# Kernel optimization log

Hardware: AMD Instinct MI355X
Metric: run time of the kernel (lower is better)

Reference implementation:

```python
import jax, jax.numpy as jnp
import numpy as np

BETA = 0.25
EPS = 1e-10


def setup_inputs() -> dict:
    key = jax.random.key(0)
    k1, k2 = jax.random.split(key)
    x = jax.random.normal(k1, (32, 64, 64, 64), dtype=jnp.float32)  # [B, C=embed_dim, H, W]
    embeddings = jax.random.normal(k2, (64, 512), dtype=jnp.float32)  # [embed_dim, K]
    return {"x": x, "embeddings": embeddings}


def reference(x, embeddings):
    B, C, H, W = x.shape
    K = embeddings.shape[1]
    sg = jax.lax.stop_gradient

    z_e = jnp.transpose(x, (0, 2, 3, 1))          # [B, H, W, C]
    z_flat = z_e.reshape(-1, C)                    # [N, C]

    # Squared L2 distances to codebook: ||z||^2 + ||e||^2 - 2 z.e
    dists = (
        jnp.sum(z_flat * z_flat, axis=1, keepdims=True)
        + jnp.sum(embeddings * embeddings, axis=0)
        - 2.0 * (z_flat @ embeddings)
    )                                              # [N, K]
    idx = jnp.argmin(dists, axis=1)                # [N]

    # Direct gather instead of one-hot matmul (same math)
    quantized = embeddings.T[idx].reshape(z_e.shape)  # [B, H, W, C]

    e_latent_loss = jnp.mean((sg(quantized) - z_e) ** 2)
    q_latent_loss = jnp.mean((quantized - sg(z_e)) ** 2)
    loss = q_latent_loss + BETA * e_latent_loss

    # Straight-through estimator
    quantized_st = z_e + sg(quantized - z_e)

    # Perplexity via codebook usage histogram (== mean of one-hot encodings)
    N = idx.shape[0]
    counts = jnp.zeros((K,), dtype=jnp.float32).at[idx].add(1.0)
    avg_probs = counts / N
    perplexity = jnp.exp(-jnp.sum(avg_probs * jnp.log(avg_probs + EPS)))

    quantized_out = jnp.transpose(quantized_st, (0, 3, 1, 2))  # [B, C, H, W]
    encoding_indices = idx.reshape(B, H, W)
    return loss, quantized_out, perplexity, encoding_indices
```

## Files before the change

kernel.cpp:

```cpp
#include <hip/hip_runtime.h>


#define B_ 32
#define C_ 64
#define HW_ 4096
#define K_ 512
#define N_ (B_ * HW_)
#define NC_ ((long long)N_ * C_)
#define ROWS_ 64
#define NBLK_ (N_ / ROWS_)
#define HBLK_ 64

typedef __attribute__((ext_vector_type(8))) short short8;
typedef __attribute__((ext_vector_type(4))) float float4_t;


__device__ __forceinline__ unsigned short f2bf(float f) {
    unsigned u = __float_as_uint(f);
    u += 0x7fffu + ((u >> 16) & 1u);
    return (unsigned short)(u >> 16);
}
__device__ __forceinline__ float bf2f(unsigned short h) {
    return __uint_as_float(((unsigned)h) << 16);
}
__device__ __forceinline__ int offA(int r, int c) {
    return ((r >> 4) << 10) + ((c >> 3) << 7) + ((r & 15) << 3) + (c & 7);
}
__device__ __forceinline__ void merge2(float& m1, int& i1, float& m2,
                                       float om1, int oi1, float om2) {
    if (om1 < m1) { m2 = fminf(m1, om2); m1 = om1; i1 = oi1; }
    else          { m2 = fminf(m2, om1); }
}

__global__ __launch_bounds__(512) void vq_init(const float* __restrict__ emb,
                                               float* __restrict__ snmax_p,
                                               float* __restrict__ en,
                                               float* __restrict__ embT32,
                                               unsigned short* __restrict__ fBhi,
                                               unsigned short* __restrict__ fBlo) {
    __shared__ float smax[8];
    int k = threadIdx.x;
    if (blockIdx.x < 64) {
        int c = blockIdx.x;
        float e = emb[c * K_ + k];
        embT32[k * C_ + c] = e;
        float s = -2.0f * e;
        unsigned short hi = f2bf(s);
        unsigned short lo = f2bf(s - bf2f(hi));
        int kk   = c >> 5;
        int lane = (((c & 31) >> 3) << 4) + (k & 15);
        int fb   = ((k >> 5) << 2) + (((k >> 4) & 1) << 1) + kk;
        int off  = (fb << 9) + (lane << 3) + (c & 7);
        fBhi[off] = hi;
        fBlo[off] = lo;
    } else {
        float s = 0.f;
#pragma unroll
        for (int c = 0; c < C_; ++c) {
            float e = emb[c * K_ + k];
            s += e * e;
        }
        en[k] = s;
        float m = s;
#pragma unroll
        for (int off = 32; off > 0; off >>= 1)
            m = fmaxf(m, __shfl_down(m, off, 64));
        if ((k & 63) == 0) smax[k >> 6] = m;
        __syncthreads();
        if (k == 0) {
            float mm = smax[0];
#pragma unroll
            for (int w2 = 1; w2 < 8; ++w2) mm = fmaxf(mm, smax[w2]);
            *snmax_p = 4.0f * mm;
        }
    }
}

__global__ __launch_bounds__(256) void vq_argmin(const float* __restrict__ x,
                                                 const float* __restrict__ en_g,
                                                 const float* __restrict__ embT32,
                                                 const unsigned short* __restrict__ fBhi,
                                                 const unsigned short* __restrict__ fBlo,
                                                 const float* __restrict__ snmax_p,
                                                 float* __restrict__ out_q,
                                                 float* __restrict__ out_idx,
                                                 double* __restrict__ ssepart) {
    __shared__ unsigned short Ast[ROWS_ * C_];
    __shared__ float sEn[K_];
    __shared__ float znp[4 * ROWS_];
    __shared__ int   biarr[ROWS_];
    __shared__ int   flaglist[ROWS_];
    __shared__ float wsse[4];
    __shared__ int   nflag;

    const int t   = threadIdx.x;
    const int n0  = blockIdx.x * ROWS_;
    const int b   = n0 >> 12;
    const int hw0 = n0 & 4095;
    const float* xbase = x + ((size_t)b << 18) + hw0;

    if (t == 0) nflag = 0;
    sEn[t]       = en_g[t];
    sEn[256 + t] = en_g[256 + t];

    float v[16];
    float znacc = 0.f;
#pragma unroll
    for (int i = 0; i < 16; ++i) {
        int id = (i << 8) + t;
        int c = id >> 6;
        int r = id & 63;
        float val = xbase[((size_t)c << 12) + r];
        v[i] = val;
        znacc += val * val;
        Ast[offA(r, c)] = f2bf(val);
    }
    znp[((t >> 6) << 6) + (t & 63)] = znacc;
    __syncthreads();

    const int lane = t & 63;
    const int w    = t >> 6;
    const int ln15 = lane & 15;
    const int quad = lane >> 4;
    const float snm = *snmax_p;

    const int ab = (w << 10) + (quad << 7) + (ln15 << 3);
    short8 ah0 = *(const short8*)(Ast + ab);
    short8 ah1 = *(const short8*)(Ast + ab + 512);
    __syncthreads();

#pragma unroll
    for (int i = 0; i < 16; ++i) {
        int id = (i << 8) + t;
        int c = id >> 6;
        int r = id & 63;
        float val = v[i];
        unsigned short hi = f2bf(val);
        Ast[offA(r, c)] = f2bf(val - bf2f(hi));
    }
    __syncthreads();
    short8 al0 = *(const short8*)(Ast + ab);
    short8 al1 = *(const short8*)(Ast + ab + 512);

    float m1[4], m2[4];
    int   i1[4];
#pragma unroll
    for (int reg = 0; reg < 4; ++reg) {
        m1[reg] = 3.4e38f; m2[reg] = 3.4e38f; i1[reg] = 0;
    }

    for (int p = 0; p < 16; ++p) {
#pragma unroll
        for (int ct = 0; ct < 2; ++ct) {
            const int fbase = ((((p << 2) + (ct << 1)) << 9) + (lane << 3));
            short8 bh0 = *(const short8*)(fBhi + fbase);
            short8 bh1 = *(const short8*)(fBhi + fbase + 512);
            short8 bl0 = *(const short8*)(fBlo + fbase);
            short8 bl1 = *(const short8*)(fBlo + fbase + 512);
            float env = sEn[(p << 5) + (ct << 4) + ln15];
            int   idx = (p << 5) + (ct << 4) + ln15;
            float4_t a0 = {0.f, 0.f, 0.f, 0.f};
            float4_t a1 = {0.f, 0.f, 0.f, 0.f};
            a0 = __builtin_amdgcn_mfma_f32_16x16x32_bf16(al0, bh0, a0, 0, 0, 0);
            a1 = __builtin_amdgcn_mfma_f32_16x16x32_bf16(al1, bh1, a1, 0, 0, 0);
            a0 = __builtin_amdgcn_mfma_f32_16x16x32_bf16(ah0, bl0, a0, 0, 0, 0);
            a1 = __builtin_amdgcn_mfma_f32_16x16x32_bf16(ah1, bl1, a1, 0, 0, 0);
            a0 = __builtin_amdgcn_mfma_f32_16x16x32_bf16(ah0, bh0, a0, 0, 0, 0);
            a1 = __builtin_amdgcn_mfma_f32_16x16x32_bf16(ah1, bh1, a1, 0, 0, 0);
#pragma unroll
            for (int reg = 0; reg < 4; ++reg) {
                float vv = (a0[reg] + a1[reg]) + env;
                if (vv < m1[reg]) {
                    m2[reg] = m1[reg]; m1[reg] = vv; i1[reg] = idx;
                } else {
                    m2[reg] = fminf(m2[reg], vv);
                }
            }
        }
    }

#pragma unroll
    for (int reg = 0; reg < 4; ++reg) {
        float a1v = m1[reg], a2v = m2[reg];
        int   ai  = i1[reg];
#pragma unroll
        for (int s = 1; s < 16; s <<= 1) {
            float o1 = __shfl_xor(a1v, s, 16);
            int   oi = __shfl_xor(ai, s, 16);
            float o2 = __shfl_xor(a2v, s, 16);
            merge2(a1v, ai, a2v, o1, oi, o2);
        }
        if (ln15 == 0) {
            int row = (w << 4) + (quad << 2) + reg;
            float znr = znp[row] + znp[64 + row] + znp[128 + row] + znp[192 + row];
            float W = 1.4e-4f * __builtin_sqrtf(znr * snm) + 1e-3f;
            biarr[row] = ai;
            if (a2v > a1v + W) {
                out_idx[n0 + row] = (float)ai;
            } else {
                int pos = atomicAdd(&nflag, 1);
                flaglist[pos] = row;
            }
        }
    }
    __syncthreads();

    int nf = nflag;
    for (int f = w; f < nf; f += 4) {
        int r = flaglist[f];
        float zl = xbase[((size_t)lane << 12) + r];
        float d[8];
#pragma unroll
        for (int j = 0; j < 8; ++j) d[j] = 0.f;
        for (int c4 = 0; c4 < 16; ++c4) {
            float z0 = __shfl(zl, (c4 << 2) + 0, 64);
            float z1 = __shfl(zl, (c4 << 2) + 1, 64);
            float z2 = __shfl(zl, (c4 << 2) + 2, 64);
            float z3 = __shfl(zl, (c4 << 2) + 3, 64);
#pragma unroll
            for (int j = 0; j < 8; ++j) {
                float4_t e = *(const float4_t*)(embT32 + ((((lane << 3) + j) << 6) + (c4 << 2)));
                d[j] = fmaf(z0, e[0], d[j]);
                d[j] = fmaf(z1, e[1], d[j]);
                d[j] = fmaf(z2, e[2], d[j]);
                d[j] = fmaf(z3, e[3], d[j]);
            }
        }
        float znr = znp[r] + znp[64 + r] + znp[128 + r] + znp[192 + r];
        float best = 3.4e38f;
        int   bidx = 0;
#pragma unroll
        for (int j = 0; j < 8; ++j) {
            int k = (lane << 3) + j;
            float dist = (znr + sEn[k]) - 2.f * d[j];
            if (dist < best) { best = dist; bidx = k; }
        }
#pragma unroll
        for (int off = 32; off > 0; off >>= 1) {
            float ov = __shfl_down(best, off, 64);
            int   oi = __shfl_down(bidx, off, 64);
            if (ov < best || (ov == best && oi < bidx)) { best = ov; bidx = oi; }
        }
        if (lane == 0) {
            biarr[r] = bidx;
            out_idx[n0 + r] = (float)bidx;
        }
    }
    __syncthreads();

    const int myrow = (w << 4) + ln15;
    const int code  = biarr[myrow];
    const float* eb = embT32 + (code << 6) + (quad << 3);
    float4_t e0 = *(const float4_t*)(eb);
    float4_t e1 = *(const float4_t*)(eb + 4);
    float4_t e2 = *(const float4_t*)(eb + 32);
    float4_t e3 = *(const float4_t*)(eb + 36);
    float* qrow = out_q + ((size_t)b << 18) + hw0 + myrow;
    float sacc = 0.f;
#pragma unroll
    for (int j = 0; j < 4; ++j) {
        int c0 = (quad << 3) + j;
        int c1 = (quad << 3) + 4 + j;
        float zA = bf2f((unsigned short)ah0[j])     + bf2f((unsigned short)al0[j]);
        float zB = bf2f((unsigned short)ah0[4 + j]) + bf2f((unsigned short)al0[4 + j]);
        float dA = e0[j] - zA, dB = e1[j] - zB;
        sacc += dA * dA + dB * dB;
        qrow[(size_t)c0 << 12] = e0[j];
        qrow[(size_t)c1 << 12] = e1[j];
        float zC = bf2f((unsigned short)ah1[j])     + bf2f((unsigned short)al1[j]);
        float zD = bf2f((unsigned short)ah1[4 + j]) + bf2f((unsigned short)al1[4 + j]);
        float dC = e2[j] - zC, dD = e3[j] - zD;
        sacc += dC * dC + dD * dD;
        qrow[(size_t)(32 + c0) << 12] = e2[j];
        qrow[(size_t)(32 + c1) << 12] = e3[j];
    }
#pragma unroll
    for (int off = 32; off > 0; off >>= 1)
        sacc += __shfl_down(sacc, off, 64);
    if (lane == 0) wsse[w] = sacc;
    __syncthreads();
    if (t == 0)
        ssepart[blockIdx.x] = (double)wsse[0] + (double)wsse[1]
                            + (double)wsse[2] + (double)wsse[3];
}

__global__ __launch_bounds__(256) void vq_hist(const float* __restrict__ out_idx,
                                               int* __restrict__ histpart) {
    __shared__ int h[K_];
    int t = threadIdx.x;
    h[t] = 0; h[t + 256] = 0;
    __syncthreads();
    const float* ip = out_idx + blockIdx.x * (N_ / HBLK_);
#pragma unroll
    for (int i = 0; i < (N_ / HBLK_) / 256; ++i) {
        int k = (int)ip[(i << 8) + t];
        atomicAdd(&h[k], 1);
    }
    __syncthreads();
    histpart[blockIdx.x * K_ + t]       = h[t];
    histpart[blockIdx.x * K_ + 256 + t] = h[t + 256];
}

__global__ __launch_bounds__(512) void vq_final(const int* __restrict__ histpart,
                                                const double* __restrict__ ssepart,
                                                float* __restrict__ out_loss,
                                                float* __restrict__ out_perp) {
    __shared__ float  wsf[8];
    __shared__ double wsd[8];
    int t = threadIdx.x;
    int hsum = 0;
#pragma unroll 8
    for (int b = 0; b < HBLK_; ++b)
        hsum += histpart[b * K_ + t];
    float p = (float)hsum / (float)N_;
    float s = p * logf(p + 1e-10f);
    double d = ssepart[t] + ssepart[t + 512] + ssepart[t + 1024] + ssepart[t + 1536];
#pragma unroll
    for (int off = 32; off > 0; off >>= 1) {
        s += __shfl_down(s, off, 64);
        d += __shfl_down(d, off, 64);
    }
    if ((t & 63) == 0) { wsf[t >> 6] = s; wsd[t >> 6] = d; }
    __syncthreads();
    if (t == 0) {
        float  S = 0.f;
        double D = 0.0;
#pragma unroll
        for (int w = 0; w < 8; ++w) { S += wsf[w]; D += wsd[w]; }
        *out_perp = expf(-S);
        *out_loss = (float)(1.25 * D / (double)NC_);
    }
}

extern "C" void kernel_launch(void* const* d_in, const int* in_sizes, int n_in,
                              void* d_out, int out_size, void* d_ws, size_t ws_size,
                              hipStream_t stream) {
    const float* x   = (const float*)d_in[0];
    const float* emb = (const float*)d_in[1];

    float* out      = (float*)d_out;
    float* out_loss = out;
    float* out_q    = out + 1;
    float* out_perp = out + 1 + (size_t)N_ * C_;
    float* out_idx  = out + 2 + (size_t)N_ * C_;

    char* ws = (char*)d_ws;
    float*          snmax_p  = (float*)(ws + 56);
    float*          en       = (float*)(ws + 2112);
    float*          embT32   = (float*)(ws + 4160);
    unsigned short* fBhi     = (unsigned short*)(ws + 135232);
    unsigned short* fBlo     = (unsigned short*)(ws + 200768);
    int*            histpart = (int*)(ws + 135232);
    double*         ssepart  = (double*)(ws + 266304);

    vq_init<<<65, 512, 0, stream>>>(emb, snmax_p, en, embT32, fBhi, fBlo);
    vq_argmin<<<NBLK_, 256, 0, stream>>>(x, en, embT32, fBhi, fBlo, snmax_p,
                                         out_q, out_idx, ssepart);
    vq_hist<<<HBLK_, 256, 0, stream>>>(out_idx, histpart);
    vq_final<<<1, 512, 0, stream>>>(histpart, ssepart, out_loss, out_perp);
}
```

Measured before the change: 154.6 us.

## Fuse histogram and final reduction into argmin kernel via last-block pattern

Removes the separate histogram and finalize kernels. Each block now atomically accumulates its SSE into a global double, and the last block to finish builds the codebook histogram and writes loss and perplexity. The MFMA loop is also restructured to prefetch the next codebook fragments a step ahead, adds a fourth lo*lo product term, seeds the accumulator with the codebook norms, and tightens the ambiguity margin so fewer rows fall back to exact fp32 rescoring. The cost is a serial tail where one block scans all 131072 indices, plus an extra MFMA per tile.

Measured after the change: 337.4 us. 2.18x slower.

```diff
diff --git a/kernel.cpp b/kernel.cpp
--- a/kernel.cpp
+++ b/kernel.cpp
@@ -9,7 +9,6 @@
 #define NC_ ((long long)N_ * C_)
 #define ROWS_ 64
 #define NBLK_ (N_ / ROWS_)
-#define HBLK_ 64
 
 typedef __attribute__((ext_vector_type(8))) short short8;
 typedef __attribute__((ext_vector_type(4))) float float4_t;
@@ -33,6 +32,8 @@
 }
 
 __global__ __launch_bounds__(512) void vq_init(const float* __restrict__ emb,
+                                               double* __restrict__ sse,
+                                               int* __restrict__ done,
                                                float* __restrict__ snmax_p,
                                                float* __restrict__ en,
                                                float* __restrict__ embT32,
@@ -54,6 +55,7 @@
         fBhi[off] = hi;
         fBlo[off] = lo;
     } else {
+        if (k == 0) { *sse = 0.0; *done = 0; }
         float s = 0.f;
 #pragma unroll
         for (int c = 0; c < C_; ++c) {
@@ -76,22 +78,27 @@
     }
 }
 
-__global__ __launch_bounds__(256) void vq_argmin(const float* __restrict__ x,
-                                                 const float* __restrict__ en_g,
-                                                 const float* __restrict__ embT32,
-                                                 const unsigned short* __restrict__ fBhi,
-                                                 const unsigned short* __restrict__ fBlo,
-                                                 const float* __restrict__ snmax_p,
-                                                 float* __restrict__ out_q,
-                                                 float* __restrict__ out_idx,
-                                                 double* __restrict__ ssepart) {
+__global__ __launch_bounds__(256) void vq_fused(const float* __restrict__ x,
+                                                const float* __restrict__ en_g,
+                                                const float* __restrict__ embT32,
+                                                const unsigned short* __restrict__ fBhi,
+                                                const unsigned short* __restrict__ fBlo,
+                                                const float* __restrict__ snmax_p,
+                                                float* __restrict__ out_q,
+                                                float* __restrict__ out_idx,
+                                                float* __restrict__ out_loss,
+                                                float* __restrict__ out_perp,
+                                                double* __restrict__ sse_g,
+                                                int* __restrict__ done) {
     __shared__ unsigned short Ast[ROWS_ * C_];
     __shared__ float sEn[K_];
     __shared__ float znp[4 * ROWS_];
     __shared__ int   biarr[ROWS_];
     __shared__ int   flaglist[ROWS_];
+    __shared__ int   h[K_];
     __shared__ float wsse[4];
     __shared__ int   nflag;
+    __shared__ int   islast;
 
     const int t   = threadIdx.x;
     const int n0  = blockIdx.x * ROWS_;
@@ -149,32 +156,40 @@
         m1[reg] = 3.4e38f; m2[reg] = 3.4e38f; i1[reg] = 0;
     }
 
-    for (int p = 0; p < 16; ++p) {
-#pragma unroll
-        for (int ct = 0; ct < 2; ++ct) {
-            const int fbase = ((((p << 2) + (ct << 1)) << 9) + (lane << 3));
-            short8 bh0 = *(const short8*)(fBhi + fbase);
-            short8 bh1 = *(const short8*)(fBhi + fbase + 512);
-            short8 bl0 = *(const short8*)(fBlo + fbase);
-            short8 bl1 = *(const short8*)(fBlo + fbase + 512);
-            float env = sEn[(p << 5) + (ct << 4) + ln15];
-            int   idx = (p << 5) + (ct << 4) + ln15;
-            float4_t a0 = {0.f, 0.f, 0.f, 0.f};
-            float4_t a1 = {0.f, 0.f, 0.f, 0.f};
-            a0 = __builtin_amdgcn_mfma_f32_16x16x32_bf16(al0, bh0, a0, 0, 0, 0);
-            a1 = __builtin_amdgcn_mfma_f32_16x16x32_bf16(al1, bh1, a1, 0, 0, 0);
-            a0 = __builtin_amdgcn_mfma_f32_16x16x32_bf16(ah0, bl0, a0, 0, 0, 0);
-            a1 = __builtin_amdgcn_mfma_f32_16x16x32_bf16(ah1, bl1, a1, 0, 0, 0);
-            a0 = __builtin_amdgcn_mfma_f32_16x16x32_bf16(ah0, bh0, a0, 0, 0, 0);
-            a1 = __builtin_amdgcn_mfma_f32_16x16x32_bf16(ah1, bh1, a1, 0, 0, 0);
-#pragma unroll
-            for (int reg = 0; reg < 4; ++reg) {
-                float vv = (a0[reg] + a1[reg]) + env;
-                if (vv < m1[reg]) {
-                    m2[reg] = m1[reg]; m1[reg] = vv; i1[reg] = idx;
-                } else {
-                    m2[reg] = fminf(m2[reg], vv);
-                }
+    short8 nb0 = *(const short8*)(fBhi + (lane << 3));
+    short8 nb1 = *(const short8*)(fBhi + (lane << 3) + 512);
+    short8 nb2 = *(const short8*)(fBlo + (lane << 3));
+    short8 nb3 = *(const short8*)(fBlo + (lane << 3) + 512);
+
+#pragma unroll 2
+    for (int it = 0; it < 32; ++it) {
+        short8 bh0 = nb0, bh1 = nb1, bl0 = nb2, bl1 = nb3;
+        if (it < 31) {
+            const int nfb = ((it + 1) << 10) + (lane << 3);
+            nb0 = *(const short8*)(fBhi + nfb);
+            nb1 = *(const short8*)(fBhi + nfb + 512);
+            nb2 = *(const short8*)(fBlo + nfb);
+            nb3 = *(const short8*)(fBlo + nfb + 512);
+        }
+        float env = sEn[(it << 4) + ln15];
+        int   idx = (it << 4) + ln15;
+        float4_t a0 = {env, env, env, env};
+        float4_t a1 = {0.f, 0.f, 0.f, 0.f};
+        a0 = __builtin_amdgcn_mfma_f32_16x16x32_bf16(al0, bl0, a0, 0, 0, 0);
+        a1 = __builtin_amdgcn_mfma_f32_16x16x32_bf16(al1, bl1, a1, 0, 0, 0);
+        a0 = __builtin_amdgcn_mfma_f32_16x16x32_bf16(al0, bh0, a0, 0, 0, 0);
+        a1 = __builtin_amdgcn_mfma_f32_16x16x32_bf16(al1, bh1, a1, 0, 0, 0);
+        a0 = __builtin_amdgcn_mfma_f32_16x16x32_bf16(ah0, bl0, a0, 0, 0, 0);
+        a1 = __builtin_amdgcn_mfma_f32_16x16x32_bf16(ah1, bl1, a1, 0, 0, 0);
+        a0 = __builtin_amdgcn_mfma_f32_16x16x32_bf16(ah0, bh0, a0, 0, 0, 0);
+        a1 = __builtin_amdgcn_mfma_f32_16x16x32_bf16(ah1, bh1, a1, 0, 0, 0);
+#pragma unroll
+        for (int reg = 0; reg < 4; ++reg) {
+            float vv = a0[reg] + a1[reg];
+            if (vv < m1[reg]) {
+                m2[reg] = m1[reg]; m1[reg] = vv; i1[reg] = idx;
+            } else {
+                m2[reg] = fminf(m2[reg], vv);
             }
         }
     }
@@ -193,10 +208,12 @@
         if (ln15 == 0) {
             int row = (w << 4) + (quad << 2) + reg;
             float znr = znp[row] + znp[64 + row] + znp[128 + row] + znp[192 + row];
-            float W = 1.4e-4f * __builtin_sqrtf(znr * snm) + 1e-3f;
+            float S = __builtin_sqrtf(znr * snm);
+            float W = 6.5e-5f * S + 3e-6f * (znr + snm) + 1e-4f;
             biarr[row] = ai;
             if (a2v > a1v + W) {
-                out_idx[n0 + row] = (float)ai;
+                __hip_atomic_store(&out_idx[n0 + row], (float)ai,
+                                   __ATOMIC_RELAXED, __HIP_MEMORY_SCOPE_AGENT);
             } else {
                 int pos = atomicAdd(&nflag, 1);
                 flaglist[pos] = row;
@@ -243,7 +260,8 @@
         }
         if (lane == 0) {
             biarr[r] = bidx;
-            out_idx[n0 + r] = (float)bidx;
+            __hip_atomic_store(&out_idx[n0 + r], (float)bidx,
+                               __ATOMIC_RELAXED, __HIP_MEMORY_SCOPE_AGENT);
         }
     }
     __syncthreads();
@@ -279,56 +297,42 @@
         sacc += __shfl_down(sacc, off, 64);
     if (lane == 0) wsse[w] = sacc;
     __syncthreads();
-    if (t == 0)
-        ssepart[blockIdx.x] = (double)wsse[0] + (double)wsse[1]
-                            + (double)wsse[2] + (double)wsse[3];
-}
-
-__global__ __launch_bounds__(256) void vq_hist(const float* __restrict__ out_idx,
-                                               int* __restrict__ histpart) {
-    __shared__ int h[K_];
-    int t = threadIdx.x;
-    h[t] = 0; h[t + 256] = 0;
-    __syncthreads();
-    const float* ip = out_idx + blockIdx.x * (N_ / HBLK_);
-#pragma unroll
-    for (int i = 0; i < (N_ / HBLK_) / 256; ++i) {
-        int k = (int)ip[(i << 8) + t];
-        atomicAdd(&h[k], 1);
-    }
-    __syncthreads();
-    histpart[blockIdx.x * K_ + t]       = h[t];
-    histpart[blockIdx.x * K_ + 256 + t] = h[t + 256];
-}
-
-__global__ __launch_bounds__(512) void vq_final(const int* __restrict__ histpart,
-                                                const double* __restrict__ ssepart,
-                                                float* __restrict__ out_loss,
-                                                float* __restrict__ out_perp) {
-    __shared__ float  wsf[8];
-    __shared__ double wsd[8];
-    int t = threadIdx.x;
-    int hsum = 0;
-#pragma unroll 8
-    for (int b = 0; b < HBLK_; ++b)
-        hsum += histpart[b * K_ + t];
-    float p = (float)hsum / (float)N_;
-    float s = p * logf(p + 1e-10f);
-    double d = ssepart[t] + ssepart[t + 512] + ssepart[t + 1024] + ssepart[t + 1536];
-#pragma unroll
-    for (int off = 32; off > 0; off >>= 1) {
-        s += __shfl_down(s, off, 64);
-        d += __shfl_down(d, off, 64);
-    }
-    if ((t & 63) == 0) { wsf[t >> 6] = s; wsd[t >> 6] = d; }
-    __syncthreads();
+
     if (t == 0) {
-        float  S = 0.f;
-        double D = 0.0;
-#pragma unroll
-        for (int w = 0; w < 8; ++w) { S += wsf[w]; D += wsd[w]; }
-        *out_perp = expf(-S);
-        *out_loss = (float)(1.25 * D / (double)NC_);
+        double bs = (double)wsse[0] + (double)wsse[1]
+                  + (double)wsse[2] + (double)wsse[3];
+        atomicAdd(sse_g, bs);
+        __threadfence();
+        islast = (atomicAdd(done, 1) == NBLK_ - 1);
+    }
+    __syncthreads();
+    if (islast) {
+        __threadfence();
+        h[t] = 0; h[t + 256] = 0;
+        __syncthreads();
+        for (int i = 0; i < N_ / 256; ++i) {
+            float fv = __hip_atomic_load(&out_idx[(i << 8) + t],
+                                         __ATOMIC_RELAXED, __HIP_MEMORY_SCOPE_AGENT);
+            atomicAdd(&h[(int)fv], 1);
+        }
+        __syncthreads();
+        float s = 0.f;
+#pragma unroll
+        for (int j = 0; j < 2; ++j) {
+            float pp = (float)h[t + (j << 8)] / (float)N_;
+            s += pp * logf(pp + 1e-10f);
+        }
+#pragma unroll
+        for (int off = 32; off > 0; off >>= 1)
+            s += __shfl_down(s, off, 64);
+        if (lane == 0) wsse[w] = s;
+        __syncthreads();
+        if (t == 0) {
+            float S2 = wsse[0] + wsse[1] + wsse[2] + wsse[3];
+            double sv = atomicAdd(sse_g, 0.0);
+            out_perp[0] = expf(-S2);
+            out_loss[0] = (float)(1.25 * sv / (double)NC_);
+        }
     }
 }
 
@@ -345,17 +349,16 @@
     float* out_idx  = out + 2 + (size_t)N_ * C_;
 
     char* ws = (char*)d_ws;
-    float*          snmax_p  = (float*)(ws + 56);
-    float*          en       = (float*)(ws + 2112);
-    float*          embT32   = (float*)(ws + 4160);
-    unsigned short* fBhi     = (unsigned short*)(ws + 135232);
-    unsigned short* fBlo     = (unsigned short*)(ws + 200768);
-    int*            histpart = (int*)(ws + 135232);
-    double*         ssepart  = (double*)(ws + 266304);
-
-    vq_init<<<65, 512, 0, stream>>>(emb, snmax_p, en, embT32, fBhi, fBlo);
-    vq_argmin<<<NBLK_, 256, 0, stream>>>(x, en, embT32, fBhi, fBlo, snmax_p,
-                                         out_q, out_idx, ssepart);
-    vq_hist<<<HBLK_, 256, 0, stream>>>(out_idx, histpart);
-    vq_final<<<1, 512, 0, stream>>>(histpart, ssepart, out_loss, out_perp);
-}
+    double*         sse     = (double*)(ws + 0);
+    int*            done    = (int*)(ws + 8);
+    float*          snmax_p = (float*)(ws + 56);
+    float*          en      = (float*)(ws + 2112);
+    float*          embT32  = (float*)(ws + 4160);
+    unsigned short* fBhi    = (unsigned short*)(ws + 135232);
+    unsigned short* fBlo    = (unsigned short*)(ws + 200768);
+
+    vq_init<<<65, 512, 0, stream>>>(emb, sse, done, snmax_p, en, embT32, fBhi, fBlo);
+    vq_fused<<<NBLK_, 256, 0, stream>>>(x, en, embT32, fBhi, fBlo, snmax_p,
+                                        out_q, out_idx, out_loss, out_perp,
+                                        sse, done);
+}
```

## Double rows per block, stage codebook in LDS, fold histogram into tail kernel

Applied to the files above, without the earlier changes.

Each argmin block now handles 128 rows as two row tiles per wave, so every codebook fragment is reused twice. The codebook fragments are staged through a double-buffered LDS ring with register prefetch instead of being read straight from global memory. A fourth low-by-low MFMA term is added, the codebook norm is seeded into the accumulator, and the tie-break threshold is tightened. The fallback exact-distance pass reads the original embedding layout, and the separate histogram and final kernels are merged into one single-block tail kernel. The risks are a serial 131k-element histogram in that single block, more register pressure from the launch-bounds hint, and a tighter threshold that could mis-flag near-tie rows.

Result: slower. 196.2 us (+26.9%).

```diff
diff --git a/kernel.cpp b/kernel.cpp
--- a/kernel.cpp
+++ b/kernel.cpp
@@ -7,9 +7,8 @@
 #define K_ 512
 #define N_ (B_ * HW_)
 #define NC_ ((long long)N_ * C_)
-#define ROWS_ 64
+#define ROWS_ 128
 #define NBLK_ (N_ / ROWS_)
-#define HBLK_ 64
 
 typedef __attribute__((ext_vector_type(8))) short short8;
 typedef __attribute__((ext_vector_type(4))) float float4_t;
@@ -76,25 +75,26 @@
     }
 }
 
-__global__ __launch_bounds__(256) void vq_argmin(const float* __restrict__ x,
-                                                 const float* __restrict__ en_g,
-                                                 const float* __restrict__ embT32,
-                                                 const unsigned short* __restrict__ fBhi,
-                                                 const unsigned short* __restrict__ fBlo,
-                                                 const float* __restrict__ snmax_p,
-                                                 float* __restrict__ out_q,
-                                                 float* __restrict__ out_idx,
-                                                 double* __restrict__ ssepart) {
-    __shared__ unsigned short Ast[ROWS_ * C_];
+__global__ __launch_bounds__(256, 4) void vq_argmin(const float* __restrict__ x,
+                                                    const float* __restrict__ emb,
+                                                    const float* __restrict__ en_g,
+                                                    const float* __restrict__ embT32,
+                                                    const unsigned short* __restrict__ fBhi,
+                                                    const unsigned short* __restrict__ fBlo,
+                                                    const float* __restrict__ snmax_p,
+                                                    float* __restrict__ out_q,
+                                                    float* __restrict__ out_idx,
+                                                    double* __restrict__ ssepart) {
+    __shared__ unsigned short SBuf[8192];
     __shared__ float sEn[K_];
-    __shared__ float znp[4 * ROWS_];
+    __shared__ float znp[256];
     __shared__ int   biarr[ROWS_];
     __shared__ int   flaglist[ROWS_];
     __shared__ float wsse[4];
     __shared__ int   nflag;
 
     const int t   = threadIdx.x;
-    const int n0  = blockIdx.x * ROWS_;
+    const int n0  = blockIdx.x << 7;
     const int b   = n0 >> 12;
     const int hw0 = n0 & 4095;
     const float* xbase = x + ((size_t)b << 18) + hw0;
@@ -103,19 +103,19 @@
     sEn[t]       = en_g[t];
     sEn[256 + t] = en_g[256 + t];
 
-    float v[16];
+    float v[32];
     float znacc = 0.f;
 #pragma unroll
-    for (int i = 0; i < 16; ++i) {
+    for (int i = 0; i < 32; ++i) {
         int id = (i << 8) + t;
-        int c = id >> 6;
-        int r = id & 63;
+        int c = id >> 7;
+        int r = id & 127;
         float val = xbase[((size_t)c << 12) + r];
         v[i] = val;
         znacc += val * val;
-        Ast[offA(r, c)] = f2bf(val);
-    }
-    znp[((t >> 6) << 6) + (t & 63)] = znacc;
+        SBuf[offA(r, c)] = f2bf(val);
+    }
+    znp[((t >> 7) << 7) + (t & 127)] = znacc;
     __syncthreads();
 
     const int lane = t & 63;
@@ -124,115 +124,152 @@
     const int quad = lane >> 4;
     const float snm = *snmax_p;
 
-    const int ab = (w << 10) + (quad << 7) + (ln15 << 3);
-    short8 ah0 = *(const short8*)(Ast + ab);
-    short8 ah1 = *(const short8*)(Ast + ab + 512);
-    __syncthreads();
-
-#pragma unroll
-    for (int i = 0; i < 16; ++i) {
+    short8 ah[2][2], al[2][2];
+    int abof[2];
+#pragma unroll
+    for (int rtl = 0; rtl < 2; ++rtl) {
+        abof[rtl] = (((w << 1) + rtl) << 10) + (quad << 7) + (ln15 << 3);
+        ah[rtl][0] = *(const short8*)(SBuf + abof[rtl]);
+        ah[rtl][1] = *(const short8*)(SBuf + abof[rtl] + 512);
+    }
+    __syncthreads();
+
+    uint4 ph = ((const uint4*)fBhi)[t];
+    uint4 pl = ((const uint4*)fBlo)[t];
+
+#pragma unroll
+    for (int i = 0; i < 32; ++i) {
         int id = (i << 8) + t;
-        int c = id >> 6;
-        int r = id & 63;
+        int c = id >> 7;
+        int r = id & 127;
         float val = v[i];
         unsigned short hi = f2bf(val);
-        Ast[offA(r, c)] = f2bf(val - bf2f(hi));
-    }
-    __syncthreads();
-    short8 al0 = *(const short8*)(Ast + ab);
-    short8 al1 = *(const short8*)(Ast + ab + 512);
-
-    float m1[4], m2[4];
-    int   i1[4];
-#pragma unroll
-    for (int reg = 0; reg < 4; ++reg) {
-        m1[reg] = 3.4e38f; m2[reg] = 3.4e38f; i1[reg] = 0;
-    }
-
-    for (int p = 0; p < 16; ++p) {
-#pragma unroll
-        for (int ct = 0; ct < 2; ++ct) {
-            const int fbase = ((((p << 2) + (ct << 1)) << 9) + (lane << 3));
-            short8 bh0 = *(const short8*)(fBhi + fbase);
-            short8 bh1 = *(const short8*)(fBhi + fbase + 512);
-            short8 bl0 = *(const short8*)(fBlo + fbase);
-            short8 bl1 = *(const short8*)(fBlo + fbase + 512);
-            float env = sEn[(p << 5) + (ct << 4) + ln15];
-            int   idx = (p << 5) + (ct << 4) + ln15;
-            float4_t a0 = {0.f, 0.f, 0.f, 0.f};
-            float4_t a1 = {0.f, 0.f, 0.f, 0.f};
-            a0 = __builtin_amdgcn_mfma_f32_16x16x32_bf16(al0, bh0, a0, 0, 0, 0);
-            a1 = __builtin_amdgcn_mfma_f32_16x16x32_bf16(al1, bh1, a1, 0, 0, 0);
-            a0 = __builtin_amdgcn_mfma_f32_16x16x32_bf16(ah0, bl0, a0, 0, 0, 0);
-            a1 = __builtin_amdgcn_mfma_f32_16x16x32_bf16(ah1, bl1, a1, 0, 0, 0);
-            a0 = __builtin_amdgcn_mfma_f32_16x16x32_bf16(ah0, bh0, a0, 0, 0, 0);
-            a1 = __builtin_amdgcn_mfma_f32_16x16x32_bf16(ah1, bh1, a1, 0, 0, 0);
-#pragma unroll
-            for (int reg = 0; reg < 4; ++reg) {
-                float vv = (a0[reg] + a1[reg]) + env;
-                if (vv < m1[reg]) {
-                    m2[reg] = m1[reg]; m1[reg] = vv; i1[reg] = idx;
-                } else {
-                    m2[reg] = fminf(m2[reg], vv);
+        SBuf[offA(r, c)] = f2bf(val - bf2f(hi));
+    }
+    __syncthreads();
+#pragma unroll
+    for (int rtl = 0; rtl < 2; ++rtl) {
+        al[rtl][0] = *(const short8*)(SBuf + abof[rtl]);
+        al[rtl][1] = *(const short8*)(SBuf + abof[rtl] + 512);
+    }
+    __syncthreads();
+
+    {
+        uint4* dst = (uint4*)SBuf;
+        dst[t]       = ph;
+        dst[256 + t] = pl;
+    }
+    __syncthreads();
+
+    float m1[2][4], m2[2][4];
+    int   i1[2][4];
+#pragma unroll
+    for (int rtl = 0; rtl < 2; ++rtl)
+#pragma unroll
+        for (int reg = 0; reg < 4; ++reg) {
+            m1[rtl][reg] = 3.4e38f; m2[rtl][reg] = 3.4e38f; i1[rtl][reg] = 0;
+        }
+
+    for (int cch = 0; cch < 16; ++cch) {
+        const int d = cch & 1;
+        if (cch < 15) {
+            ph = ((const uint4*)fBhi)[((cch + 1) << 8) + t];
+            pl = ((const uint4*)fBlo)[((cch + 1) << 8) + t];
+        }
+        const unsigned short* Bb = SBuf + (d << 12);
+#pragma unroll
+        for (int q = 0; q < 2; ++q) {
+            const unsigned short* Bh = Bb + (q << 10);
+            const unsigned short* Bl = Bb + 2048 + (q << 10);
+            short8 bh0 = *(const short8*)(Bh + (lane << 3));
+            short8 bh1 = *(const short8*)(Bh + 512 + (lane << 3));
+            short8 bl0 = *(const short8*)(Bl + (lane << 3));
+            short8 bl1 = *(const short8*)(Bl + 512 + (lane << 3));
+            const int it  = (cch << 1) + q;
+            const float env = sEn[(it << 4) + ln15];
+            const int   idx = (it << 4) + ln15;
+#pragma unroll
+            for (int rtl = 0; rtl < 2; ++rtl) {
+                float4_t a0 = {env, env, env, env};
+                float4_t a1 = {0.f, 0.f, 0.f, 0.f};
+                a0 = __builtin_amdgcn_mfma_f32_16x16x32_bf16(al[rtl][0], bl0, a0, 0, 0, 0);
+                a1 = __builtin_amdgcn_mfma_f32_16x16x32_bf16(al[rtl][1], bl1, a1, 0, 0, 0);
+                a0 = __builtin_amdgcn_mfma_f32_16x16x32_bf16(al[rtl][0], bh0, a0, 0, 0, 0);
+                a1 = __builtin_amdgcn_mfma_f32_16x16x32_bf16(al[rtl][1], bh1, a1, 0, 0, 0);
+                a0 = __builtin_amdgcn_mfma_f32_16x16x32_bf16(ah[rtl][0], bl0, a0, 0, 0, 0);
+                a1 = __builtin_amdgcn_mfma_f32_16x16x32_bf16(ah[rtl][1], bl1, a1, 0, 0, 0);
+                a0 = __builtin_amdgcn_mfma_f32_16x16x32_bf16(ah[rtl][0], bh0, a0, 0, 0, 0);
+                a1 = __builtin_amdgcn_mfma_f32_16x16x32_bf16(ah[rtl][1], bh1, a1, 0, 0, 0);
+#pragma unroll
+                for (int reg = 0; reg < 4; ++reg) {
+                    float vv = a0[reg] + a1[reg];
+                    if (vv < m1[rtl][reg]) {
+                        m2[rtl][reg] = m1[rtl][reg]; m1[rtl][reg] = vv; i1[rtl][reg] = idx;
+                    } else {
+                        m2[rtl][reg] = fminf(m2[rtl][reg], vv);
+                    }
                 }
             }
         }
-    }
-
-#pragma unroll
-    for (int reg = 0; reg < 4; ++reg) {
-        float a1v = m1[reg], a2v = m2[reg];
-        int   ai  = i1[reg];
-#pragma unroll
-        for (int s = 1; s < 16; s <<= 1) {
-            float o1 = __shfl_xor(a1v, s, 16);
-            int   oi = __shfl_xor(ai, s, 16);
-            float o2 = __shfl_xor(a2v, s, 16);
-            merge2(a1v, ai, a2v, o1, oi, o2);
-        }
-        if (ln15 == 0) {
-            int row = (w << 4) + (quad << 2) + reg;
-            float znr = znp[row] + znp[64 + row] + znp[128 + row] + znp[192 + row];
-            float W = 1.4e-4f * __builtin_sqrtf(znr * snm) + 1e-3f;
-            biarr[row] = ai;
-            if (a2v > a1v + W) {
-                out_idx[n0 + row] = (float)ai;
-            } else {
-                int pos = atomicAdd(&nflag, 1);
-                flaglist[pos] = row;
+        __syncthreads();
+        if (cch < 15) {
+            uint4* dst = (uint4*)SBuf + ((d ^ 1) << 9);
+            dst[t]       = ph;
+            dst[256 + t] = pl;
+        }
+        __syncthreads();
+    }
+
+#pragma unroll
+    for (int rtl = 0; rtl < 2; ++rtl)
+#pragma unroll
+        for (int reg = 0; reg < 4; ++reg) {
+            float a1v = m1[rtl][reg], a2v = m2[rtl][reg];
+            int   ai  = i1[rtl][reg];
+#pragma unroll
+            for (int s = 1; s < 16; s <<= 1) {
+                float o1 = __shfl_xor(a1v, s, 16);
+                int   oi = __shfl_xor(ai, s, 16);
+                float o2 = __shfl_xor(a2v, s, 16);
+                merge2(a1v, ai, a2v, o1, oi, o2);
             }
-        }
-    }
+            if (ln15 == 0) {
+                int row = (((w << 1) + rtl) << 4) + (quad << 2) + reg;
+                float znr = znp[row] + znp[128 + row];
+                float S = __builtin_sqrtf(znr * snm);
+                float W = 6.5e-5f * S + 3e-6f * (znr + snm) + 1e-4f;
+                biarr[row] = ai;
+                if (a2v > a1v + W) {
+                    out_idx[n0 + row] = (float)ai;
+                } else {
+                    int pos = atomicAdd(&nflag, 1);
+                    flaglist[pos] = row;
+                }
+            }
+        }
     __syncthreads();
 
     int nf = nflag;
     for (int f = w; f < nf; f += 4) {
         int r = flaglist[f];
         float zl = xbase[((size_t)lane << 12) + r];
-        float d[8];
-#pragma unroll
-        for (int j = 0; j < 8; ++j) d[j] = 0.f;
-        for (int c4 = 0; c4 < 16; ++c4) {
-            float z0 = __shfl(zl, (c4 << 2) + 0, 64);
-            float z1 = __shfl(zl, (c4 << 2) + 1, 64);
-            float z2 = __shfl(zl, (c4 << 2) + 2, 64);
-            float z3 = __shfl(zl, (c4 << 2) + 3, 64);
-#pragma unroll
-            for (int j = 0; j < 8; ++j) {
-                float4_t e = *(const float4_t*)(embT32 + ((((lane << 3) + j) << 6) + (c4 << 2)));
-                d[j] = fmaf(z0, e[0], d[j]);
-                d[j] = fmaf(z1, e[1], d[j]);
-                d[j] = fmaf(z2, e[2], d[j]);
-                d[j] = fmaf(z3, e[3], d[j]);
-            }
-        }
-        float znr = znp[r] + znp[64 + r] + znp[128 + r] + znp[192 + r];
+        float dd[8];
+#pragma unroll
+        for (int j = 0; j < 8; ++j) dd[j] = 0.f;
+        for (int c = 0; c < C_; ++c) {
+            float zc = __shfl(zl, c, 64);
+            const float* ep = emb + (c << 9);
+#pragma unroll
+            for (int j = 0; j < 8; ++j)
+                dd[j] = fmaf(zc, ep[(j << 6) + lane], dd[j]);
+        }
+        float znr = znp[r] + znp[128 + r];
         float best = 3.4e38f;
         int   bidx = 0;
 #pragma unroll
         for (int j = 0; j < 8; ++j) {
-            int k = (lane << 3) + j;
-            float dist = (znr + sEn[k]) - 2.f * d[j];
+            int k = (j << 6) + lane;
+            float dist = (znr + sEn[k]) - 2.f * dd[j];
             if (dist < best) { best = dist; bidx = k; }
         }
 #pragma unroll
@@ -248,31 +285,34 @@
     }
     __syncthreads();
 
-    const int myrow = (w << 4) + ln15;
-    const int code  = biarr[myrow];
-    const float* eb = embT32 + (code << 6) + (quad << 3);
-    float4_t e0 = *(const float4_t*)(eb);
-    float4_t e1 = *(const float4_t*)(eb + 4);
-    float4_t e2 = *(const float4_t*)(eb + 32);
-    float4_t e3 = *(const float4_t*)(eb + 36);
-    float* qrow = out_q + ((size_t)b << 18) + hw0 + myrow;
     float sacc = 0.f;
 #pragma unroll
-    for (int j = 0; j < 4; ++j) {
-        int c0 = (quad << 3) + j;
-        int c1 = (quad << 3) + 4 + j;
-        float zA = bf2f((unsigned short)ah0[j])     + bf2f((unsigned short)al0[j]);
-        float zB = bf2f((unsigned short)ah0[4 + j]) + bf2f((unsigned short)al0[4 + j]);
-        float dA = e0[j] - zA, dB = e1[j] - zB;
-        sacc += dA * dA + dB * dB;
-        qrow[(size_t)c0 << 12] = e0[j];
-        qrow[(size_t)c1 << 12] = e1[j];
-        float zC = bf2f((unsigned short)ah1[j])     + bf2f((unsigned short)al1[j]);
-        float zD = bf2f((unsigned short)ah1[4 + j]) + bf2f((unsigned short)al1[4 + j]);
-        float dC = e2[j] - zC, dD = e3[j] - zD;
-        sacc += dC * dC + dD * dD;
-        qrow[(size_t)(32 + c0) << 12] = e2[j];
-        qrow[(size_t)(32 + c1) << 12] = e3[j];
+    for (int rtl = 0; rtl < 2; ++rtl) {
+        const int myrow = (((w << 1) + rtl) << 4) + ln15;
+        const int code  = biarr[myrow];
+        const float* eb = embT32 + (code << 6) + (quad << 3);
+        float4_t e0 = *(const float4_t*)(eb);
+        float4_t e1 = *(const float4_t*)(eb + 4);
+        float4_t e2 = *(const float4_t*)(eb + 32);
+        float4_t e3 = *(const float4_t*)(eb + 36);
+        float* qrow = out_q + ((size_t)b << 18) + hw0 + myrow;
+#pragma unroll
+        for (int j = 0; j < 4; ++j) {
+            int c0 = (quad << 3) + j;
+            int c1 = (quad << 3) + 4 + j;
+            float zA = bf2f((unsigned short)ah[rtl][0][j])     + bf2f((unsigned short)al[rtl][0][j]);
+            float zB = bf2f((unsigned short)ah[rtl][0][4 + j]) + bf2f((unsigned short)al[rtl][0][4 + j]);
+            float dA = e0[j] - zA, dB = e1[j] - zB;
+            sacc += dA * dA + dB * dB;
+            qrow[(size_t)c0 << 12] = e0[j];
+            qrow[(size_t)c1 << 12] = e1[j];
+            float zC = bf2f((unsigned short)ah[rtl][1][j])     + bf2f((unsigned short)al[rtl][1][j]);
+            float zD = bf2f((unsigned short)ah[rtl][1][4 + j]) + bf2f((unsigned short)al[rtl][1][4 + j]);
+            float dC = e2[j] - zC, dD = e3[j] - zD;
+            sacc += dC * dC + dD * dD;
+            qrow[(size_t)(32 + c0) << 12] = e2[j];
+            qrow[(size_t)(32 + c1) << 12] = e3[j];
+        }
     }
 #pragma unroll
     for (int off = 32; off > 0; off >>= 1)
@@ -284,37 +324,25 @@
                             + (double)wsse[2] + (double)wsse[3];
 }
 
-__global__ __launch_bounds__(256) void vq_hist(const float* __restrict__ out_idx,
-                                               int* __restrict__ histpart) {
-    __shared__ int h[K_];
-    int t = threadIdx.x;
-    h[t] = 0; h[t + 256] = 0;
-    __syncthreads();
-    const float* ip = out_idx + blockIdx.x * (N_ / HBLK_);
-#pragma unroll
-    for (int i = 0; i < (N_ / HBLK_) / 256; ++i) {
-        int k = (int)ip[(i << 8) + t];
-        atomicAdd(&h[k], 1);
-    }
-    __syncthreads();
-    histpart[blockIdx.x * K_ + t]       = h[t];
-    histpart[blockIdx.x * K_ + 256 + t] = h[t + 256];
-}
-
-__global__ __launch_bounds__(512) void vq_final(const int* __restrict__ histpart,
-                                                const double* __restrict__ ssepart,
-                                                float* __restrict__ out_loss,
-                                                float* __restrict__ out_perp) {
+__global__ __launch_bounds__(512) void vq_tail(const float* __restrict__ out_idx,
+                                               const double* __restrict__ ssepart,
+                                               float* __restrict__ out_loss,
+                                               float* __restrict__ out_perp) {
+    __shared__ int    h[K_];
     __shared__ float  wsf[8];
     __shared__ double wsd[8];
     int t = threadIdx.x;
-    int hsum = 0;
+    h[t] = 0;
+    __syncthreads();
 #pragma unroll 8
-    for (int b = 0; b < HBLK_; ++b)
-        hsum += histpart[b * K_ + t];
-    float p = (float)hsum / (float)N_;
+    for (int i = 0; i < N_ / 512; ++i) {
+        int k = (int)out_idx[(i << 9) + t];
+        atomicAdd(&h[k], 1);
+    }
+    __syncthreads();
+    float p = (float)h[t] / (float)N_;
     float s = p * logf(p + 1e-10f);
-    double d = ssepart[t] + ssepart[t + 512] + ssepart[t + 1024] + ssepart[t + 1536];
+    double d = ssepart[t] + ssepart[512 + t];
 #pragma unroll
     for (int off = 32; off > 0; off >>= 1) {
         s += __shfl_down(s, off, 64);
@@ -345,17 +373,15 @@
     float* out_idx  = out + 2 + (size_t)N_ * C_;
 
     char* ws = (char*)d_ws;
-    float*          snmax_p  = (float*)(ws + 56);
-    float*          en       = (float*)(ws + 2112);
-    float*          embT32   = (float*)(ws + 4160);
-    unsigned short* fBhi     = (unsigned short*)(ws + 135232);
-    unsigned short* fBlo     = (unsigned short*)(ws + 200768);
-    int*            histpart = (int*)(ws + 135232);
-    double*         ssepart  = (double*)(ws + 266304);
+    float*          snmax_p = (float*)(ws + 56);
+    float*          en      = (float*)(ws + 2112);
+    float*          embT32  = (float*)(ws + 4160);
+    unsigned short* fBhi    = (unsigned short*)(ws + 135232);
+    unsigned short* fBlo    = (unsigned short*)(ws + 200768);
+    double*         ssepart = (double*)(ws + 266304);
 
     vq_init<<<65, 512, 0, stream>>>(emb, snmax_p, en, embT32, fBhi, fBlo);
-    vq_argmin<<<NBLK_, 256, 0, stream>>>(x, en, embT32, fBhi, fBlo, snmax_p,
+    vq_argmin<<<NBLK_, 256, 0, stream>>>(x, emb, en, embT32, fBhi, fBlo, snmax_p,
                                          out_q, out_idx, ssepart);
-    vq_hist<<<HBLK_, 256, 0, stream>>>(out_idx, histpart);
-    vq_final<<<1, 512, 0, stream>>>(histpart, ssepart, out_loss, out_perp);
-}
+    vq_tail<<<1, 512, 0, stream>>>(out_idx, ssepart, out_loss, out_perp);
+}
```
